# Optimization experiments

Hardware: AMD Instinct MI355X
Metric: run time of the kernel (lower is better)

## Reference

```python
import jax, jax.numpy as jnp
import numpy as np

B, S, D = 4, 2048, 512
H = 8
DEPTH = D // H  # 64


def setup_inputs() -> dict:
    key = jax.random.key(0)
    ks = jax.random.split(key, 6)
    scale = 1.0 / np.sqrt(D)
    return {
        "x": jax.random.normal(ks[0], (B, S, D), dtype=jnp.float32),
        "y": jax.random.normal(ks[1], (B, S, D), dtype=jnp.float32),
        "W_q": jax.random.normal(ks[2], (D, D), dtype=jnp.float32) * scale,
        "W_k": jax.random.normal(ks[3], (D, D), dtype=jnp.float32) * scale,
        "W_v": jax.random.normal(ks[4], (D, D), dtype=jnp.float32) * scale,
        "W_o": jax.random.normal(ks[5], (D, D), dtype=jnp.float32) * scale,
    }


def _split_heads(t):
    # [B, S, D] -> [B, H, S, DEPTH]
    b, s, _ = t.shape
    return t.reshape(b, s, H, DEPTH).transpose(0, 2, 1, 3)


def reference(x, y, W_q, W_k, W_v, W_o):
    q = _split_heads(x @ W_q) * (DEPTH ** -0.5)   # [B,H,Sq,d]
    k = _split_heads(y @ W_k)                      # [B,H,Sk,d]
    v = _split_heads(y @ W_v)                      # [B,H,Sk,d]
    logits = jnp.einsum("bhqd,bhkd->bhqk", q, k)   # [B,H,Sq,Sk]
    weights = jax.nn.softmax(logits, axis=-1)
    attn = jnp.einsum("bhqk,bhkd->bhqd", weights, v)  # [B,H,Sq,d]
    attn = attn.transpose(0, 2, 1, 3).reshape(x.shape[0], x.shape[1], D)
    return attn @ W_o
```

## Files before the change

### kernel.cpp

```cpp
#include <hip/hip_runtime.h>
#include <hip/hip_bf16.h>
#include <math.h>
#include <stdint.h>

#define NB 4
#define NS 2048
#define ND 512
#define NH 8
#define DEP 64
#define KVHALF (NS / 2)

typedef __attribute__((ext_vector_type(8))) short bf16x8;
typedef __attribute__((ext_vector_type(4))) short bf16x4;
typedef __attribute__((ext_vector_type(4))) float f32x4;
typedef __attribute__((ext_vector_type(16))) float f32x16;

#define QSCALE 0.18033688011112042f

__device__ __forceinline__ short f2b(float f) {
  unsigned u = __float_as_uint(f);
  u += 0x7FFF + ((u >> 16) & 1);
  return (short)(u >> 16);
}
__device__ __forceinline__ unsigned pk2(float a, float b) {
  union { __hip_bfloat162 h; unsigned u; } c;
  c.h = __float22bfloat162_rn(float2{a, b});
  return c.u;
}
__device__ __forceinline__ void dma16(const void* g, void* l) {
  __builtin_amdgcn_global_load_lds(
      (const __attribute__((address_space(1))) void*)g,
      (__attribute__((address_space(3))) void*)l, 16, 0, 0);
}

__global__ __launch_bounds__(256) void prep(
    const float* __restrict__ x, const float* __restrict__ y,
    const float* __restrict__ W0, const float* __restrict__ W1,
    const float* __restrict__ W2, const float* __restrict__ W3,
    short* __restrict__ xb, short* __restrict__ yb, short* __restrict__ T0,
    short* __restrict__ T1, short* __restrict__ T2, short* __restrict__ T3) {
  const int t = threadIdx.x;
  if (blockIdx.y < 2) {
    const float* src = blockIdx.y ? y : x;
    short* dst = blockIdx.y ? yb : xb;
    size_t i = ((size_t)blockIdx.x * 256 + t) * 4;
    float4 v = *(const float4*)(src + i);
    bf16x4 o;
    o[0] = f2b(v.x); o[1] = f2b(v.y); o[2] = f2b(v.z); o[3] = f2b(v.w);
    *(bf16x4*)(dst + i) = o;
    return;
  }
  const int bx = blockIdx.x;
  if (bx >= 256) return;
  const int wj = bx >> 6, rem = bx & 63;
  const float* W = wj == 0 ? W0 : wj == 1 ? W1 : wj == 2 ? W2 : W3;
  short* T = wj == 0 ? T0 : wj == 1 ? T1 : wj == 2 ? T2 : T3;
  __shared__ float tile[64][65];
  const int k0 = (rem >> 3) * 64, n0 = (rem & 7) * 64;
#pragma unroll
  for (int i = 0; i < 4; ++i) {
    int r = (t >> 4) + i * 16;
    int c = (t & 15) * 4;
    float4 v = *(const float4*)&W[(size_t)(k0 + r) * ND + n0 + c];
    tile[r][c] = v.x; tile[r][c + 1] = v.y;
    tile[r][c + 2] = v.z; tile[r][c + 3] = v.w;
  }
  __syncthreads();
#pragma unroll
  for (int i = 0; i < 4; ++i) {
    int n = (t >> 4) + i * 16;
    int kc = (t & 15) * 4;
    bf16x4 o;
#pragma unroll
    for (int j = 0; j < 4; ++j) o[j] = f2b(tile[kc + j][n]);
    *(bf16x4*)&T[(size_t)(n0 + n) * ND + k0 + kc] = o;
  }
}

__device__ __forceinline__ void gemm128(const short* __restrict__ A,
                                        const short* __restrict__ Bt,
                                        short* __restrict__ Cout, int mode,
                                        float alpha) {
  __shared__ short As[128 * 64];
  __shared__ short Bs[128 * 64];
  __shared__ short Tb[64 * 128];
  const int t = threadIdx.x;
  const int wave = t >> 6, lane = t & 63;
  const int m = lane & 15, quad = lane >> 4;
  const int m0 = blockIdx.y * 128, n0 = blockIdx.x * 128;
  const int mh = (wave >> 1) * 64, nh = (wave & 1) * 64;
  const int r8 = lane >> 3;
  const int c8 = (lane & 7) ^ r8;
  const int mx7 = m & 7;
  f32x4 acc[4][4];
#pragma unroll
  for (int i = 0; i < 4; ++i)
#pragma unroll
    for (int j = 0; j < 4; ++j) acc[i][j] = (f32x4){0.f, 0.f, 0.f, 0.f};

  for (int k0 = 0; k0 < ND; k0 += 64) {
    __syncthreads();
#pragma unroll
    for (int i = 0; i < 4; ++i) {
      int row = i * 32 + wave * 8 + r8;
      dma16(A + (size_t)(m0 + row) * ND + k0 + c8 * 8,
            As + (i * 256 + wave * 64) * 8);
      dma16(Bt + (size_t)(n0 + row) * ND + k0 + c8 * 8,
            Bs + (i * 256 + wave * 64) * 8);
    }
    __syncthreads();
    bf16x8 af[4][2], bf[4][2];
#pragma unroll
    for (int mt = 0; mt < 4; ++mt)
#pragma unroll
      for (int kc = 0; kc < 2; ++kc)
        af[mt][kc] = *(const bf16x8*)(As + (mh + mt * 16 + m) * 64 +
                                      ((kc * 4 + quad) ^ mx7) * 8);
#pragma unroll
    for (int nt = 0; nt < 4; ++nt)
#pragma unroll
      for (int kc = 0; kc < 2; ++kc)
        bf[nt][kc] = *(const bf16x8*)(Bs + (nh + nt * 16 + m) * 64 +
                                      ((kc * 4 + quad) ^ mx7) * 8);
#pragma unroll
    for (int mt = 0; mt < 4; ++mt)
#pragma unroll
      for (int nt = 0; nt < 4; ++nt)
#pragma unroll
        for (int kc = 0; kc < 2; ++kc)
          acc[mt][nt] = __builtin_amdgcn_mfma_f32_16x16x32_bf16(
              af[mt][kc], bf[nt][kc], acc[mt][nt], 0, 0, 0);
  }
  if (mode == 2) {
    const int h0 = n0 >> 6;
    const int b_ = m0 >> 11, s0g = m0 & (NS - 1);
#pragma unroll
    for (int p = 0; p < 2; ++p) {
      __syncthreads();
      if ((wave & 1) == p) {
#pragma unroll
        for (int mt = 0; mt < 4; ++mt)
#pragma unroll
          for (int nt = 0; nt < 4; ++nt)
#pragma unroll
            for (int r = 0; r < 4; ++r)
              Tb[(nt * 16 + m) * 128 + mh + mt * 16 + quad * 4 + r] =
                  f2b(acc[mt][nt][r] * alpha);
      }
      __syncthreads();
      {
        int c = t >> 2, sc = (t & 3) * 32;
        int gcol = p * 64 + c;
        int h_ = h0 + (gcol >> 6), d_ = gcol & (DEP - 1);
        short* dst =
            Cout + (size_t)((b_ * NH + h_) * DEP + d_) * NS + s0g + sc;
        const short* src = Tb + c * 128 + sc;
#pragma unroll
        for (int i = 0; i < 4; ++i)
          *(bf16x8*)(dst + i * 8) = *(const bf16x8*)(src + i * 8);
      }
    }
  } else {
#pragma unroll
    for (int mt = 0; mt < 4; ++mt)
#pragma unroll
      for (int nt = 0; nt < 4; ++nt)
#pragma unroll
        for (int r = 0; r < 4; ++r) {
          int row = m0 + mh + mt * 16 + quad * 4 + r;
          int col = n0 + nh + nt * 16 + m;
          Cout[(size_t)row * ND + col] = f2b(acc[mt][nt][r] * alpha);
        }
  }
}

__global__ __launch_bounds__(256) void qkv_gemm(
    const short* __restrict__ xb, const short* __restrict__ yb,
    const short* __restrict__ Wqt, const short* __restrict__ Wkt,
    const short* __restrict__ Wvt, short* __restrict__ Qb,
    short* __restrict__ Kb, short* __restrict__ Vtb) {
  if (blockIdx.z == 0)
    gemm128(xb, Wqt, Qb, 1, QSCALE);
  else if (blockIdx.z == 1)
    gemm128(yb, Wkt, Kb, 1, 1.0f);
  else
    gemm128(yb, Wvt, Vtb, 2, 1.0f);
}

__global__ __launch_bounds__(256) void out_gemm(const short* __restrict__ A,
                                                const short* __restrict__ Bt,
                                                float* __restrict__ Cout) {
  __shared__ short As[2][128 * 64];
  __shared__ short Bs[2][64 * 64];
  const int t = threadIdx.x;
  const int wave = t >> 6, lane = t & 63;
  const int m = lane & 15, quad = lane >> 4;
  const int m0 = blockIdx.y * 128, n0 = blockIdx.x * 64;
  const int mh = (wave >> 1) * 64, nh = (wave & 1) * 32;
  const int r8 = lane >> 3;
  const int c8 = (lane & 7) ^ r8;
  const int mx7 = m & 7;
  f32x4 acc[4][2];
#pragma unroll
  for (int i = 0; i < 4; ++i)
#pragma unroll
    for (int j = 0; j < 2; ++j) acc[i][j] = (f32x4){0.f, 0.f, 0.f, 0.f};

#pragma unroll
  for (int i = 0; i < 4; ++i)
    dma16(A + (size_t)(m0 + i * 32 + wave * 8 + r8) * ND + c8 * 8,
          As[0] + (i * 256 + wave * 64) * 8);
#pragma unroll
  for (int i = 0; i < 2; ++i)
    dma16(Bt + (size_t)(n0 + i * 32 + wave * 8 + r8) * ND + c8 * 8,
          Bs[0] + (i * 256 + wave * 64) * 8);

  int buf = 0;
  for (int k0 = 0; k0 < ND; k0 += 64, buf ^= 1) {
    __syncthreads();
    if (k0 + 64 < ND) {
#pragma unroll
      for (int i = 0; i < 4; ++i)
        dma16(A + (size_t)(m0 + i * 32 + wave * 8 + r8) * ND + k0 + 64 + c8 * 8,
              As[buf ^ 1] + (i * 256 + wave * 64) * 8);
#pragma unroll
      for (int i = 0; i < 2; ++i)
        dma16(Bt + (size_t)(n0 + i * 32 + wave * 8 + r8) * ND + k0 + 64 +
                  c8 * 8,
              Bs[buf ^ 1] + (i * 256 + wave * 64) * 8);
    }
    bf16x8 af[4][2], bf[2][2];
#pragma unroll
    for (int mt = 0; mt < 4; ++mt)
#pragma unroll
      for (int kc = 0; kc < 2; ++kc)
        af[mt][kc] = *(const bf16x8*)(As[buf] + (mh + mt * 16 + m) * 64 +
                                      ((kc * 4 + quad) ^ mx7) * 8);
#pragma unroll
    for (int nt = 0; nt < 2; ++nt)
#pragma unroll
      for (int kc = 0; kc < 2; ++kc)
        bf[nt][kc] = *(const bf16x8*)(Bs[buf] + (nh + nt * 16 + m) * 64 +
                                      ((kc * 4 + quad) ^ mx7) * 8);
#pragma unroll
    for (int mt = 0; mt < 4; ++mt)
#pragma unroll
      for (int nt = 0; nt < 2; ++nt)
#pragma unroll
        for (int kc = 0; kc < 2; ++kc)
          acc[mt][nt] = __builtin_amdgcn_mfma_f32_16x16x32_bf16(
              af[mt][kc], bf[nt][kc], acc[mt][nt], 0, 0, 0);
  }
#pragma unroll
  for (int mt = 0; mt < 4; ++mt)
#pragma unroll
    for (int nt = 0; nt < 2; ++nt)
#pragma unroll
      for (int r = 0; r < 4; ++r) {
        int row = m0 + mh + mt * 16 + quad * 4 + r;
        int col = n0 + nh + nt * 16 + m;
        Cout[(size_t)row * ND + col] = acc[mt][nt][r];
      }
}

__global__ __launch_bounds__(512, 4) void attn_mfma(
    const short* __restrict__ Qb, const short* __restrict__ Kb,
    const short* __restrict__ Vtb, short* __restrict__ Ob) {
  __shared__ short Ks[2][2][64 * 64];
  __shared__ short Vts[2][2][64 * 64];
  const int t = threadIdx.x;
  const int wave = t >> 6, lane = t & 63;
  const int zh = wave >> 2, wl = wave & 3;
  const int l31 = lane & 31, hi = lane >> 5;
  const int sw = lane & 7;
  const int bh = blockIdx.y, b = bh >> 3, h = bh & 7;
  const int q0 = blockIdx.x * 128 + wl * 32;
  const int kvb = zh * KVHALF;
  const size_t rowb = (size_t)b * NS;
  const short* Vtbase = Vtb + (size_t)(bh * DEP) * NS;
  const int r8 = lane >> 3;
  const int c8 = (lane & 7) ^ r8;

  bf16x8 qf[4];
#pragma unroll
  for (int dc = 0; dc < 4; ++dc)
    qf[dc] = *(const bf16x8*)(Qb + (rowb + q0 + l31) * ND + h * DEP + dc * 16 +
                              hi * 8);

  f32x16 kzero;
#pragma unroll
  for (int i = 0; i < 16; ++i) kzero[i] = 0.f;

  float l_ = 0.0f;
  f32x16 Ot[2];
#pragma unroll
  for (int dt = 0; dt < 2; ++dt)
#pragma unroll
    for (int i = 0; i < 16; ++i) Ot[dt][i] = 0.f;

#pragma unroll
  for (int i = 0; i < 2; ++i) {
    int row = i * 32 + wl * 8 + r8;
    dma16(Kb + (rowb + kvb + row) * ND + h * DEP + c8 * 8,
          &Ks[zh][0][(i * 256 + wl * 64) * 8]);
    dma16(Vtbase + (size_t)row * NS + kvb + c8 * 8,
          &Vts[zh][0][(i * 256 + wl * 64) * 8]);
  }

  int buf = 0;
  for (int kv0 = 0; kv0 < KVHALF; kv0 += 64, buf ^= 1) {
    __syncthreads();
    if (kv0 + 64 < KVHALF) {
#pragma unroll
      for (int i = 0; i < 2; ++i) {
        int row = i * 32 + wl * 8 + r8;
        dma16(Kb + (rowb + kvb + kv0 + 64 + row) * ND + h * DEP + c8 * 8,
              &Ks[zh][buf ^ 1][(i * 256 + wl * 64) * 8]);
        dma16(Vtbase + (size_t)row * NS + kvb + kv0 + 64 + c8 * 8,
              &Vts[zh][buf ^ 1][(i * 256 + wl * 64) * 8]);
      }
    }

    f32x16 St[2];
#pragma unroll
    for (int kt = 0; kt < 2; ++kt) {
      bf16x8 kf0 = *(const bf16x8*)(&Ks[zh][buf][(kt * 32 + l31) * 64 +
                                                 (hi ^ sw) * 8]);
      St[kt] = __builtin_amdgcn_mfma_f32_32x32x16_bf16(kf0, qf[0], kzero,
                                                       0, 0, 0);
#pragma unroll
      for (int dc = 1; dc < 4; ++dc) {
        bf16x8 kf = *(const bf16x8*)(&Ks[zh][buf][(kt * 32 + l31) * 64 +
                                                  ((dc * 2 + hi) ^ sw) * 8]);
        St[kt] = __builtin_amdgcn_mfma_f32_32x32x16_bf16(kf, qf[dc], St[kt],
                                                         0, 0, 0);
      }
    }

    bf16x8 pf[4];
    float rs = 0.f;
#pragma unroll
    for (int s = 0; s < 4; ++s) {
      const int kt = s >> 1, base = (s & 1) * 8;
      float E[8];
#pragma unroll
      for (int j = 0; j < 8; ++j) {
        E[j] = __builtin_amdgcn_exp2f(St[kt][base + j]);
      }
      rs += ((E[0] + E[1]) + (E[2] + E[3])) + ((E[4] + E[5]) + (E[6] + E[7]));
      unsigned A0 = pk2(E[0], E[1]), A1 = pk2(E[2], E[3]);
      unsigned A2 = pk2(E[4], E[5]), A3 = pk2(E[6], E[7]);
      auto r02 =
          __builtin_amdgcn_permlane32_swap((int)A0, (int)A2, false, false);
      auto r13 =
          __builtin_amdgcn_permlane32_swap((int)A1, (int)A3, false, false);
      union { bf16x8 v; int u[4]; } pu;
      pu.u[0] = r02[0]; pu.u[1] = r13[0]; pu.u[2] = r02[1]; pu.u[3] = r13[1];
      pf[s] = pu.v;
    }
    l_ += rs;

#pragma unroll
    for (int dt = 0; dt < 2; ++dt)
#pragma unroll
      for (int s = 0; s < 4; ++s) {
        bf16x8 vf = *(const bf16x8*)(&Vts[zh][buf][(dt * 32 + l31) * 64 +
                                                   ((s * 2 + hi) ^ sw) * 8]);
        Ot[dt] = __builtin_amdgcn_mfma_f32_32x32x16_bf16(vf, pf[s], Ot[dt],
                                                         0, 0, 0);
      }
  }

  l_ += __shfl_xor(l_, 32, 64);

  __syncthreads();
  float* Ox = (float*)Ks;
  float* lx = (float*)Vts;
  if (zh == 1) {
#pragma unroll
    for (int dt = 0; dt < 2; ++dt)
#pragma unroll
      for (int r = 0; r < 16; ++r) {
        int d = dt * 32 + (r & 3) + 8 * (r >> 2) + 4 * hi;
        Ox[(wl * 64 + d) * 32 + l31] = Ot[dt][r];
      }
    if (lane < 32) lx[wl * 32 + l31] = l_;
  }
  __syncthreads();
  if (zh == 0) {
    float linv = 1.0f / (l_ + lx[wl * 32 + l31]);
    size_t row = rowb + q0 + l31;
#pragma unroll
    for (int dt = 0; dt < 2; ++dt)
#pragma unroll
      for (int g = 0; g < 4; ++g) {
        int d0 = dt * 32 + g * 8 + hi * 4;
        float o[4];
#pragma unroll
        for (int j = 0; j < 4; ++j)
          o[j] = Ot[dt][g * 4 + j] + Ox[(wl * 64 + d0 + j) * 32 + l31];
        uint2 pk;
        pk.x = pk2(o[0] * linv, o[1] * linv);
        pk.y = pk2(o[2] * linv, o[3] * linv);
        *(uint2*)(Ob + row * ND + h * DEP + d0) = pk;
      }
  }
}

extern "C" void kernel_launch(void* const* d_in, const int* in_sizes, int n_in,
                              void* d_out, int out_size, void* d_ws,
                              size_t ws_size, hipStream_t stream) {
  const float* x = (const float*)d_in[0];
  const float* y = (const float*)d_in[1];
  const float* Wq = (const float*)d_in[2];
  const float* Wk = (const float*)d_in[3];
  const float* Wv = (const float*)d_in[4];
  const float* Wo = (const float*)d_in[5];
  float* out = (float*)d_out;

  const size_t mat = (size_t)NB * NS * ND;
  const size_t wsz = (size_t)ND * ND;
  short* xb = (short*)d_ws;
  short* yb = xb + mat;
  short* Wqt = yb + mat;
  short* Wkt = Wqt + wsz;
  short* Wvt = Wkt + wsz;
  short* Wot = Wvt + wsz;
  short* Qb = Wot + wsz;
  short* Kb = Qb + mat;
  short* Vtb = Kb + mat;
  short* attnb = xb;

  prep<<<dim3(mat / 1024, 3), 256, 0, stream>>>(x, y, Wq, Wk, Wv, Wo, xb, yb,
                                                Wqt, Wkt, Wvt, Wot);
  qkv_gemm<<<dim3(ND / 128, (NB * NS) / 128, 3), 256, 0, stream>>>(
      xb, yb, Wqt, Wkt, Wvt, Qb, Kb, Vtb);
  attn_mfma<<<dim3(NS / 128, NB * NH), 512, 0, stream>>>(Qb, Kb, Vtb, attnb);
  out_gemm<<<dim3(ND / 64, (NB * NS) / 128), 256, 0, stream>>>(attnb, Wot,
                                                               out);
}
```

Before: 184.1 us.

## Drop K/V double buffering to halve LDS footprint for higher occupancy

Replaces the double-buffered K/V shared-memory tiles with a single buffer per half, loading each tile synchronously between two barriers. A small separate array holds the row-sum reduction scratch. This halves LDS use per block so more blocks can be resident per CU. The cost is losing the prefetch overlap of the next tile's loads with the current tile's MFMA work, plus an extra barrier per iteration.

```diff
diff --git a/kernel.cpp b/kernel.cpp
--- a/kernel.cpp
+++ b/kernel.cpp
@@ -266,8 +266,8 @@
 __global__ __launch_bounds__(512, 4) void attn_mfma(
     const short* __restrict__ Qb, const short* __restrict__ Kb,
     const short* __restrict__ Vtb, short* __restrict__ Ob) {
-  __shared__ short Ks[2][2][64 * 64];
-  __shared__ short Vts[2][2][64 * 64];
+  __shared__ short KVs[2][2][64 * 64];
+  __shared__ float lxs[128];
   const int t = threadIdx.x;
   const int wave = t >> 6, lane = t & 63;
   const int zh = wave >> 2, wl = wave & 3;
@@ -280,6 +280,8 @@
   const short* Vtbase = Vtb + (size_t)(bh * DEP) * NS;
   const int r8 = lane >> 3;
   const int c8 = (lane & 7) ^ r8;
+  short* Ksb = &KVs[0][zh][0];
+  short* Vsb = &KVs[1][zh][0];
 
   bf16x8 qf[4];
 #pragma unroll
@@ -298,40 +300,29 @@
 #pragma unroll
     for (int i = 0; i < 16; ++i) Ot[dt][i] = 0.f;
 
-#pragma unroll
-  for (int i = 0; i < 2; ++i) {
-    int row = i * 32 + wl * 8 + r8;
-    dma16(Kb + (rowb + kvb + row) * ND + h * DEP + c8 * 8,
-          &Ks[zh][0][(i * 256 + wl * 64) * 8]);
-    dma16(Vtbase + (size_t)row * NS + kvb + c8 * 8,
-          &Vts[zh][0][(i * 256 + wl * 64) * 8]);
-  }
-
-  int buf = 0;
-  for (int kv0 = 0; kv0 < KVHALF; kv0 += 64, buf ^= 1) {
+  for (int kv0 = 0; kv0 < KVHALF; kv0 += 64) {
     __syncthreads();
-    if (kv0 + 64 < KVHALF) {
-#pragma unroll
-      for (int i = 0; i < 2; ++i) {
-        int row = i * 32 + wl * 8 + r8;
-        dma16(Kb + (rowb + kvb + kv0 + 64 + row) * ND + h * DEP + c8 * 8,
-              &Ks[zh][buf ^ 1][(i * 256 + wl * 64) * 8]);
-        dma16(Vtbase + (size_t)row * NS + kvb + kv0 + 64 + c8 * 8,
-              &Vts[zh][buf ^ 1][(i * 256 + wl * 64) * 8]);
-      }
-    }
+#pragma unroll
+    for (int i = 0; i < 2; ++i) {
+      int row = i * 32 + wl * 8 + r8;
+      dma16(Kb + (rowb + kvb + kv0 + row) * ND + h * DEP + c8 * 8,
+            Ksb + (i * 256 + wl * 64) * 8);
+      dma16(Vtbase + (size_t)row * NS + kvb + kv0 + c8 * 8,
+            Vsb + (i * 256 + wl * 64) * 8);
+    }
+    __syncthreads();
 
     f32x16 St[2];
 #pragma unroll
     for (int kt = 0; kt < 2; ++kt) {
-      bf16x8 kf0 = *(const bf16x8*)(&Ks[zh][buf][(kt * 32 + l31) * 64 +
-                                                 (hi ^ sw) * 8]);
+      bf16x8 kf0 = *(const bf16x8*)(Ksb + (kt * 32 + l31) * 64 +
+                                    (hi ^ sw) * 8);
       St[kt] = __builtin_amdgcn_mfma_f32_32x32x16_bf16(kf0, qf[0], kzero,
                                                        0, 0, 0);
 #pragma unroll
       for (int dc = 1; dc < 4; ++dc) {
-        bf16x8 kf = *(const bf16x8*)(&Ks[zh][buf][(kt * 32 + l31) * 64 +
-                                                  ((dc * 2 + hi) ^ sw) * 8]);
+        bf16x8 kf = *(const bf16x8*)(Ksb + (kt * 32 + l31) * 64 +
+                                     ((dc * 2 + hi) ^ sw) * 8);
         St[kt] = __builtin_amdgcn_mfma_f32_32x32x16_bf16(kf, qf[dc], St[kt],
                                                          0, 0, 0);
       }
@@ -364,8 +355,8 @@
     for (int dt = 0; dt < 2; ++dt)
 #pragma unroll
       for (int s = 0; s < 4; ++s) {
-        bf16x8 vf = *(const bf16x8*)(&Vts[zh][buf][(dt * 32 + l31) * 64 +
-                                                   ((s * 2 + hi) ^ sw) * 8]);
+        bf16x8 vf = *(const bf16x8*)(Vsb + (dt * 32 + l31) * 64 +
+                                     ((s * 2 + hi) ^ sw) * 8);
         Ot[dt] = __builtin_amdgcn_mfma_f32_32x32x16_bf16(vf, pf[s], Ot[dt],
                                                          0, 0, 0);
       }
@@ -374,8 +365,7 @@
   l_ += __shfl_xor(l_, 32, 64);
 
   __syncthreads();
-  float* Ox = (float*)Ks;
-  float* lx = (float*)Vts;
+  float* Ox = (float*)KVs;
   if (zh == 1) {
 #pragma unroll
     for (int dt = 0; dt < 2; ++dt)
@@ -384,11 +374,11 @@
         int d = dt * 32 + (r & 3) + 8 * (r >> 2) + 4 * hi;
         Ox[(wl * 64 + d) * 32 + l31] = Ot[dt][r];
       }
-    if (lane < 32) lx[wl * 32 + l31] = l_;
+    if (lane < 32) lxs[wl * 32 + l31] = l_;
   }
   __syncthreads();
   if (zh == 0) {
-    float linv = 1.0f / (l_ + lx[wl * 32 + l31]);
+    float linv = 1.0f / (l_ + lxs[wl * 32 + l31]);
     size_t row = rowb + q0 + l31;
 #pragma unroll
     for (int dt = 0; dt < 2; ++dt)
```

After: 182.0 us. No clear change (-1.1%).
